# Performance work log

Hardware: AMD Instinct MI355X
Metric: run time of the kernel (lower is better)

## Reference

```python
import jax, jax.numpy as jnp
import numpy as np

D_MODEL = 1024
NUM_HEADS = 16
D_K = D_MODEL // NUM_HEADS
B, S = 2, 2048
NEG = -1.0e9


def setup_inputs() -> dict:
    key = jax.random.key(0)
    ks = jax.random.split(key, 10)
    inp = {
        'query': jax.random.normal(ks[0], (B, S, D_MODEL), dtype=jnp.float32),
        'key':   jax.random.normal(ks[1], (B, S, D_MODEL), dtype=jnp.float32),
        'value': jax.random.normal(ks[2], (B, S, D_MODEL), dtype=jnp.float32),
        'mask':  jax.random.randint(ks[3], (B, S, S), 0, 2, dtype=jnp.int32),
        # nn.Linear params (weight [out,in], bias [out])
        'Wq': jax.random.normal(ks[4], (D_MODEL, D_MODEL), dtype=jnp.float32) * 0.02,
        'bq': jnp.zeros((D_MODEL,), dtype=jnp.float32),
        'Wk': jax.random.normal(ks[5], (D_MODEL, D_MODEL), dtype=jnp.float32) * 0.02,
        'bk': jnp.zeros((D_MODEL,), dtype=jnp.float32),
        'Wv': jax.random.normal(ks[6], (D_MODEL, D_MODEL), dtype=jnp.float32) * 0.02,
        'bv': jnp.zeros((D_MODEL,), dtype=jnp.float32),
    }
    return inp


def reference(query, key, value, mask, Wq, bq, Wk, bk, Wv, bv):
    b = query.shape[0]
    # projections: nn.Linear -> x @ W.T + b
    Q = query @ Wq.T + bq
    K = key @ Wk.T + bk
    V = value @ Wv.T + bv
    # [B, H, S, d_k]
    Q = Q.reshape(b, -1, NUM_HEADS, D_K).transpose(0, 2, 1, 3)
    K = K.reshape(b, -1, NUM_HEADS, D_K).transpose(0, 2, 1, 3)
    V = V.reshape(b, -1, NUM_HEADS, D_K).transpose(0, 2, 1, 3)
    scale = 1.0 / np.sqrt(D_K).astype(np.float32)
    scores = jnp.einsum('bhqd,bhkd->bhqk', Q, K) * scale  # [B,H,S,S]
    scores = jnp.where(mask[:, None, :, :] == 0, NEG, scores)
    attn_weights = jax.nn.softmax(scores, axis=-1)
    out = jnp.einsum('bhqk,bhkd->bhqd', attn_weights, V)
    out = out.transpose(0, 2, 1, 3).reshape(b, -1, D_MODEL)
    return out, attn_weights
```

## Files before the change

kernel.cpp:

```cpp
#include <hip/hip_runtime.h>
#include <hip/hip_bf16.h>
#include <cstdint>
#include <cstddef>

#define S_LEN 2048
#define DM 1024
#define NEGV -1.0e9f

typedef __attribute__((ext_vector_type(8))) short bf16x8;
typedef __attribute__((ext_vector_type(4))) float f32x4;
typedef __attribute__((ext_vector_type(4))) unsigned short us4;
typedef __attribute__((ext_vector_type(4))) int i32x4;
typedef __attribute__((ext_vector_type(4))) unsigned int ui32x4;
typedef __attribute__((ext_vector_type(2))) unsigned int u32x2;

__device__ __forceinline__ unsigned short f2bf(float f) {
  unsigned int u = __float_as_uint(f);
  unsigned int r = (u + 0x7fffu + ((u >> 16) & 1u)) >> 16;
  return (unsigned short)r;
}

__device__ __forceinline__ unsigned int pack_bf2(float a, float b) {
  return (unsigned int)f2bf(a) | ((unsigned int)f2bf(b) << 16);
}

__device__ __forceinline__ void async_copy16(const void* g, void* l) {
  __builtin_amdgcn_global_load_lds((const __attribute__((address_space(1))) void*)g,
                                   (__attribute__((address_space(3))) void*)l, 16, 0, 0);
}

__global__ void cvt_kernel(const float* __restrict__ src, unsigned short* __restrict__ dst, int n4) {
  int i = blockIdx.x * blockDim.x + threadIdx.x;
  if (i >= n4) return;
  const float4 v = reinterpret_cast<const float4*>(src)[i];
  us4 o;
  o[0] = f2bf(v.x); o[1] = f2bf(v.y); o[2] = f2bf(v.z); o[3] = f2bf(v.w);
  reinterpret_cast<us4*>(dst)[i] = o;
}

__global__ __launch_bounds__(256) void maskbits_kernel(const int* __restrict__ mask,
                                                       unsigned int* __restrict__ mb) {
  const int idx = blockIdx.x * 256 + threadIdx.x;
  const int row = idx >> 6, w = idx & 63;
  const int* src = mask + (size_t)row * S_LEN + w * 32;
  unsigned int r = 0;
#pragma unroll
  for (int j = 0; j < 8; ++j) {
    const i32x4 v = *(const i32x4*)(src + j * 4);
    r |= (v[0] ? 1u : 0u) << (j * 4 + 0);
    r |= (v[1] ? 1u : 0u) << (j * 4 + 1);
    r |= (v[2] ? 1u : 0u) << (j * 4 + 2);
    r |= (v[3] ? 1u : 0u) << (j * 4 + 3);
  }
  mb[(size_t)row * 64 + w] = r;
}

__global__ __launch_bounds__(256) void proj_gemm(
    const unsigned short* __restrict__ Xq, const unsigned short* __restrict__ Wqw,
    const float* __restrict__ bq, unsigned short* __restrict__ Cq,
    const unsigned short* __restrict__ Xk, const unsigned short* __restrict__ Wkw,
    const float* __restrict__ bk, unsigned short* __restrict__ Ck,
    const unsigned short* __restrict__ Xv, const unsigned short* __restrict__ Wvw,
    const float* __restrict__ bv, unsigned short* __restrict__ Cv) {
  const unsigned short* X; const unsigned short* W; const float* bias; unsigned short* C;
  if (blockIdx.z == 0)      { X = Xq; W = Wqw; bias = bq; C = Cq; }
  else if (blockIdx.z == 1) { X = Xk; W = Wkw; bias = bk; C = Ck; }
  else                      { X = Xv; W = Wvw; bias = bv; C = Cv; }

  __shared__ unsigned short Ab[128 * 64];
  __shared__ unsigned short Bb[128 * 64];

  const int t  = threadIdx.x;
  const int wv = t >> 6, l = t & 63;
  const int lr = l & 15, lg = l >> 4;
  const int wr = wv >> 1, wc = wv & 1;
  const int m0 = blockIdx.y * 128, n0 = blockIdx.x * 128;

  const f32x4 fz = {0.f, 0.f, 0.f, 0.f};
  f32x4 acc[4][4];
#pragma unroll
  for (int m = 0; m < 4; ++m)
#pragma unroll
    for (int n = 0; n < 4; ++n) acc[m][n] = fz;

  const int srow = t >> 3;
  const int sc16 = t & 7;

  for (int kt = 0; kt < 16; ++kt) {
    const int kb = kt * 64;
#pragma unroll
    for (int it = 0; it < 4; ++it) {
      const int row = it * 32 + srow;
      const int c16 = sc16 ^ (row & 7);
      const unsigned short* gA = X + (size_t)(m0 + row) * DM + kb + c16 * 8;
      const unsigned short* gB = W + (size_t)(n0 + row) * DM + kb + c16 * 8;
      async_copy16(gA, (char*)Ab + it * 4096 + wv * 1024);
      async_copy16(gB, (char*)Bb + it * 4096 + wv * 1024);
    }
    __syncthreads();
#pragma unroll
    for (int kk = 0; kk < 2; ++kk) {
      bf16x8 af[4], bfr[4];
      const int c16 = kk * 4 + lg;
      const int sw = (c16 ^ (lr & 7)) * 16;
#pragma unroll
      for (int m = 0; m < 4; ++m) {
        const int row = wr * 64 + m * 16 + lr;
        af[m] = *(const bf16x8*)((const char*)Ab + row * 128 + sw);
      }
#pragma unroll
      for (int n = 0; n < 4; ++n) {
        const int row = wc * 64 + n * 16 + lr;
        bfr[n] = *(const bf16x8*)((const char*)Bb + row * 128 + sw);
      }
#pragma unroll
      for (int m = 0; m < 4; ++m)
#pragma unroll
        for (int n = 0; n < 4; ++n)
          acc[m][n] = __builtin_amdgcn_mfma_f32_16x16x32_bf16(af[m], bfr[n], acc[m][n], 0, 0, 0);
    }
    __syncthreads();
  }

#pragma unroll
  for (int n = 0; n < 4; ++n) {
    const int ccol = n0 + wc * 64 + n * 16 + lr;
    const float bb = bias[ccol];
#pragma unroll
    for (int m = 0; m < 4; ++m) {
      const int crow0 = m0 + wr * 64 + m * 16 + lg * 4;
#pragma unroll
      for (int j = 0; j < 4; ++j)
        C[(size_t)(crow0 + j) * DM + ccol] = f2bf(acc[m][n][j] + bb);
    }
  }
}

__global__ void transpose_bf(const unsigned short* __restrict__ src, unsigned short* __restrict__ dst) {
  __shared__ unsigned short tb[32][33];
  const int x = threadIdx.x & 31, y = threadIdx.x >> 5;
  const int bx = blockIdx.x, by = blockIdx.y;
#pragma unroll
  for (int r = 0; r < 32; r += 8)
    tb[r + y][x] = src[(size_t)(by * 32 + r + y) * DM + bx * 32 + x];
  __syncthreads();
#pragma unroll
  for (int r = 0; r < 32; r += 8)
    dst[(size_t)(bx * 32 + r + y) * 4096 + by * 32 + x] = tb[x][r + y];
}

__global__ __launch_bounds__(256) void kpack_kernel(const unsigned short* __restrict__ Kp,
                                                    unsigned short* __restrict__ Kpack) {
  const int tid = blockIdx.x * 256 + threadIdx.x;
  const int lane = tid & 63;
  const int chunk = (tid >> 6) & 1;
  const int kb = (tid >> 7) & 127;
  const int h = (tid >> 14) & 15;
  const int b = tid >> 18;
  const unsigned short* src = Kp + (size_t)(b * 2048 + kb * 16 + (lane & 15)) * 1024
                                 + h * 64 + chunk * 32 + (lane >> 4) * 8;
  unsigned short* dst = Kpack + ((size_t)((b * 16 + h) * 128 + kb) * 2 + chunk) * 512 + lane * 8;
  *(bf16x8*)dst = *(const bf16x8*)src;
}

__global__ __launch_bounds__(256) void vpack_kernel(const unsigned short* __restrict__ Vt,
                                                    unsigned short* __restrict__ Vpack) {
  const int tid = blockIdx.x * 256 + threadIdx.x;
  const int lane = tid & 63;
  const int n  = (tid >> 6) & 3;
  const int s2 = (tid >> 8) & 1;
  const int pr = (tid >> 9) & 3;
  const int w  = (tid >> 11) & 7;
  const int h  = (tid >> 14) & 15;
  const int b  = tid >> 18;
  const unsigned short* src = Vt + (size_t)(h * 64 + n * 16 + (lane & 15)) * 4096
                                 + b * 2048 + w * 256 + pr * 64 + s2 * 32 + (lane >> 4) * 8;
  const int blk = ((w * 4 + pr) * 2 + s2) * 4 + n;
  unsigned short* dst = Vpack + ((size_t)(b * 16 + h) * 256 + blk) * 512 + lane * 8;
  *(bf16x8*)dst = *(const bf16x8*)src;
}

__global__ __launch_bounds__(512, 4) void attn15_kernel(
    const unsigned short* __restrict__ Qp, const unsigned short* __restrict__ Kpk,
    const unsigned short* __restrict__ Vpk, const unsigned int* __restrict__ mbits,
    float* __restrict__ outp, float* __restrict__ attnp) {
  __shared__ float rsred[8][16];
  __shared__ float rinv16[16];
  __shared__ char uni[8][4224];

  const int bx = blockIdx.x;
  const int c  = bx & 7;
  const int s  = bx >> 3;
  const int j  = s & 3;
  const int qt = s >> 2;
  const int bh = c * 4 + j;
  const int b  = bh >> 4, h = bh & 15;
  const int q0 = qt << 4;

  const int w = threadIdx.x >> 6, l = threadIdx.x & 63;
  const int lr = l & 15, lg = l >> 4;
  const int kw0 = w << 8;

  const float scale = 0.125f;
  const f32x4 fz = {0.f, 0.f, 0.f, 0.f};

  const unsigned short* Qh = Qp + (size_t)(b * S_LEN + q0 + lr) * DM + h * 64;
  const bf16x8 qf0 = *(const bf16x8*)(Qh + lg * 8);
  const bf16x8 qf1 = *(const bf16x8*)(Qh + 32 + lg * 8);

  const unsigned short* Kw = Kpk + (size_t)((b * 16 + h) * 128 + w * 16) * 1024;

  const unsigned int* mbr = mbits + ((size_t)(b * S_LEN + q0 + lr) << 6) + (kw0 >> 5);
  const ui32x4 mwa = *(const ui32x4*)(mbr);
  const ui32x4 mwb = *(const ui32x4*)(mbr + 4);

  unsigned int pkA[16], pkB[16];
  float rs = 0.f;
#pragma unroll
  for (int i = 0; i < 16; ++i) {
    const bf16x8 ka0 = *(const bf16x8*)(Kw + i * 1024 + l * 8);
    const bf16x8 ka1 = *(const bf16x8*)(Kw + i * 1024 + 512 + l * 8);
    f32x4 sc = fz;
    sc = __builtin_amdgcn_mfma_f32_16x16x32_bf16(ka0, qf0, sc, 0, 0, 0);
    sc = __builtin_amdgcn_mfma_f32_16x16x32_bf16(ka1, qf1, sc, 0, 0, 0);
    const unsigned int wsel = (i < 8) ? mwa[i >> 1] : mwb[(i - 8) >> 1];
    const unsigned int nib = (wsel >> ((i & 1) * 16 + lg * 4)) & 15u;
    const float e0 = __expf((nib & 1u) ? sc[0] * scale : NEGV);
    const float e1 = __expf((nib & 2u) ? sc[1] * scale : NEGV);
    const float e2 = __expf((nib & 4u) ? sc[2] * scale : NEGV);
    const float e3 = __expf((nib & 8u) ? sc[3] * scale : NEGV);
    rs += (e0 + e1) + (e2 + e3);
    pkA[i] = pack_bf2(e0, e1);
    pkB[i] = pack_bf2(e2, e3);
  }
  rs += __shfl_xor(rs, 16, 64);
  rs += __shfl_xor(rs, 32, 64);
  if (l < 16) rsred[w][l] = rs;
  __syncthreads();
  if (threadIdx.x < 16) {
    float s0 = 0.f;
#pragma unroll
    for (int ww = 0; ww < 8; ++ww) s0 += rsred[ww][threadIdx.x];
    rinv16[threadIdx.x] = 1.0f / s0;
  }
  __syncthreads();

  float rv4[4];
#pragma unroll
  for (int i = 0; i < 4; ++i) rv4[i] = rinv16[(l >> 4) + 4 * i];

  float* attnB = attnp + (size_t)((b * 16 + h) * S_LEN + q0) * S_LEN + kw0;
  const unsigned short* Vw = Vpk + ((size_t)(b * 16 + h) * 256 + w * 32) * 512;
  unsigned short* pbase = (unsigned short*)uni[w];

  f32x4 oacc[4];
#pragma unroll
  for (int n = 0; n < 4; ++n) oacc[n] = fz;

#pragma unroll
  for (int pr = 0; pr < 4; ++pr) {
    const int kb = pr * 64;
    unsigned short* pb = pbase + (pr & 1) * 1056;

    bf16x8 vbr[2][4];
#pragma unroll
    for (int s2 = 0; s2 < 2; ++s2)
#pragma unroll
      for (int n = 0; n < 4; ++n)
        vbr[s2][n] = *(const bf16x8*)(Vw + (size_t)(((pr * 2 + s2) * 4) + n) * 512 + l * 8);

#pragma unroll
    for (int s2 = 0; s2 < 2; ++s2) {
      const int wi = pr * 2 + s2;
      const u32x2 wv0 = {pkA[2 * wi],     pkB[2 * wi]};
      const u32x2 wv1 = {pkA[2 * wi + 1], pkB[2 * wi + 1]};
      *(u32x2*)(pb + lr * 66 + s2 * 32 + lg * 4) = wv0;
      *(u32x2*)(pb + lr * 66 + s2 * 32 + 16 + lg * 4) = wv1;
    }
#pragma unroll
    for (int i = 0; i < 4; ++i) {
      const int row = (l >> 4) + i * 4;
      const us4 p4 = *(const us4*)(pb + row * 66 + (l & 15) * 4);
      const float rv = rv4[i];
      const f32x4 st = {__uint_as_float((unsigned)p4[0] << 16) * rv,
                        __uint_as_float((unsigned)p4[1] << 16) * rv,
                        __uint_as_float((unsigned)p4[2] << 16) * rv,
                        __uint_as_float((unsigned)p4[3] << 16) * rv};
      __builtin_nontemporal_store(st, (f32x4*)(attnB + (size_t)row * S_LEN + kb + (l & 15) * 4));
    }
#pragma unroll
    for (int s2 = 0; s2 < 2; ++s2) {
      const bf16x8 pa = *(const bf16x8*)(pb + lr * 66 + s2 * 32 + lg * 8);
#pragma unroll
      for (int n = 0; n < 4; ++n)
        oacc[n] = __builtin_amdgcn_mfma_f32_16x16x32_bf16(pa, vbr[s2][n], oacc[n], 0, 0, 0);
    }
  }

  asm volatile("s_waitcnt lgkmcnt(0)" ::: "memory");
  float* outred = (float*)uni[w];
#pragma unroll
  for (int n = 0; n < 4; ++n)
#pragma unroll
    for (int jj = 0; jj < 4; ++jj)
      outred[(lg * 4 + jj) * 64 + n * 16 + lr] = oacc[n][jj];
  __syncthreads();
  if (threadIdx.x < 256) {
    const int q = threadIdx.x >> 4;
    const int d0 = (threadIdx.x & 15) * 4;
    const float rq = rinv16[q];
    float4 o = {0.f, 0.f, 0.f, 0.f};
#pragma unroll
    for (int ww = 0; ww < 8; ++ww) {
      const f32x4 sv = *(const f32x4*)((const float*)uni[ww] + q * 64 + d0);
      o.x += sv[0]; o.y += sv[1]; o.z += sv[2]; o.w += sv[3];
    }
    o.x *= rq; o.y *= rq; o.z *= rq; o.w *= rq;
    *(float4*)(outp + (size_t)(b * S_LEN + q0 + q) * DM + h * 64 + d0) = o;
  }
}

extern "C" void kernel_launch(void* const* d_in, const int* in_sizes, int n_in,
                              void* d_out, int out_size, void* d_ws, size_t ws_size,
                              hipStream_t stream) {
  const float* query = (const float*)d_in[0];
  const float* key_  = (const float*)d_in[1];
  const float* value = (const float*)d_in[2];
  const int*   mask  = (const int*)d_in[3];
  const float* Wq = (const float*)d_in[4];
  const float* bq = (const float*)d_in[5];
  const float* Wk = (const float*)d_in[6];
  const float* bk = (const float*)d_in[7];
  const float* Wv = (const float*)d_in[8];
  const float* bv = (const float*)d_in[9];

  float* outp  = (float*)d_out;
  float* attnp = outp + (size_t)2 * S_LEN * DM;

  unsigned short* ws  = (unsigned short*)d_ws;
  unsigned short* qbf = ws;
  unsigned short* kbf = qbf + 4194304;
  unsigned short* vbf = kbf + 4194304;
  unsigned short* wqb = vbf + 4194304;
  unsigned short* wkb = wqb + 1048576;
  unsigned short* wvb = wkb + 1048576;
  unsigned short* qp  = wvb + 1048576;
  unsigned short* kp  = qp + 4194304;
  unsigned short* vp  = kp + 4194304;
  unsigned short* vt  = vp + 4194304;
  unsigned int*   mb  = (unsigned int*)(vt + 4194304);
  unsigned short* kpk = qbf;
  unsigned short* vpk = kbf;

  cvt_kernel<<<4096, 256, 0, stream>>>(query, qbf, 1048576);
  cvt_kernel<<<4096, 256, 0, stream>>>(key_,  kbf, 1048576);
  cvt_kernel<<<4096, 256, 0, stream>>>(value, vbf, 1048576);
  cvt_kernel<<<1024, 256, 0, stream>>>(Wq, wqb, 262144);
  cvt_kernel<<<1024, 256, 0, stream>>>(Wk, wkb, 262144);
  cvt_kernel<<<1024, 256, 0, stream>>>(Wv, wvb, 262144);
  maskbits_kernel<<<1024, 256, 0, stream>>>(mask, mb);

  proj_gemm<<<dim3(8, 32, 3), 256, 0, stream>>>(qbf, wqb, bq, qp,
                                                kbf, wkb, bk, kp,
                                                vbf, wvb, bv, vp);
  transpose_bf<<<dim3(32, 128), 256, 0, stream>>>(vp, vt);
  kpack_kernel<<<2048, 256, 0, stream>>>(kp, kpk);
  vpack_kernel<<<2048, 256, 0, stream>>>(vt, vpk);
  attn15_kernel<<<4096, 512, 0, stream>>>(qp, kpk, vpk, mb, outp, attnp);
}
```

Baseline: 256.4 us.

## Fuse conversion launches, remap projection grid, merge V transpose and pack

Merges the six fp32-to-bf16 conversion launches into one kernel. Remaps the projection GEMM to a 1D grid with an XCD-aware block ordering so that blocks sharing an M tile land on the same chiplet. Replaces the separate V transpose and V pack kernels with one kernel that stages a 64x64 tile in LDS and writes the packed MFMA layout directly. This removes launch overhead and one full round trip of V through global memory, in exchange for strided LDS reads in the new pack kernel.

```diff
diff --git a/kernel.cpp b/kernel.cpp
--- a/kernel.cpp
+++ b/kernel.cpp
@@ -29,13 +29,27 @@
                                    (__attribute__((address_space(3))) void*)l, 16, 0, 0);
 }
 
-__global__ void cvt_kernel(const float* __restrict__ src, unsigned short* __restrict__ dst, int n4) {
-  int i = blockIdx.x * blockDim.x + threadIdx.x;
-  if (i >= n4) return;
-  const float4 v = reinterpret_cast<const float4*>(src)[i];
+__global__ __launch_bounds__(256) void cvt_all(
+    const float* __restrict__ q, const float* __restrict__ k, const float* __restrict__ v,
+    const float* __restrict__ wq, const float* __restrict__ wk, const float* __restrict__ wv,
+    unsigned short* __restrict__ qb, unsigned short* __restrict__ kb2, unsigned short* __restrict__ vb,
+    unsigned short* __restrict__ wqb, unsigned short* __restrict__ wkb, unsigned short* __restrict__ wvb) {
+  const int gid = blockIdx.x * 256 + threadIdx.x;
+  const float* src; unsigned short* dst; int idx;
+  if (gid < 3145728) {
+    const int j = gid >> 20; idx = gid & 1048575;
+    src = (j == 0) ? q : (j == 1) ? k : v;
+    dst = (j == 0) ? qb : (j == 1) ? kb2 : vb;
+  } else {
+    const int g = gid - 3145728;
+    const int j = g >> 18; idx = g & 262143;
+    src = (j == 0) ? wq : (j == 1) ? wk : wv;
+    dst = (j == 0) ? wqb : (j == 1) ? wkb : wvb;
+  }
+  const float4 vv = reinterpret_cast<const float4*>(src)[idx];
   us4 o;
-  o[0] = f2bf(v.x); o[1] = f2bf(v.y); o[2] = f2bf(v.z); o[3] = f2bf(v.w);
-  reinterpret_cast<us4*>(dst)[i] = o;
+  o[0] = f2bf(vv.x); o[1] = f2bf(vv.y); o[2] = f2bf(vv.z); o[3] = f2bf(vv.w);
+  reinterpret_cast<us4*>(dst)[idx] = o;
 }
 
 __global__ __launch_bounds__(256) void maskbits_kernel(const int* __restrict__ mask,
@@ -62,19 +76,25 @@
     const float* __restrict__ bk, unsigned short* __restrict__ Ck,
     const unsigned short* __restrict__ Xv, const unsigned short* __restrict__ Wvw,
     const float* __restrict__ bv, unsigned short* __restrict__ Cv) {
+  const int bid = blockIdx.x;
+  const int c = bid & 7, s = bid >> 3;
+  const int n0 = (s & 7) * 128;
+  const int mzg = c * 12 + (s >> 3);
+  const int m0 = (mzg & 31) * 128;
+  const int z = mzg >> 5;
+
   const unsigned short* X; const unsigned short* W; const float* bias; unsigned short* C;
-  if (blockIdx.z == 0)      { X = Xq; W = Wqw; bias = bq; C = Cq; }
-  else if (blockIdx.z == 1) { X = Xk; W = Wkw; bias = bk; C = Ck; }
-  else                      { X = Xv; W = Wvw; bias = bv; C = Cv; }
+  if (z == 0)      { X = Xq; W = Wqw; bias = bq; C = Cq; }
+  else if (z == 1) { X = Xk; W = Wkw; bias = bk; C = Ck; }
+  else             { X = Xv; W = Wvw; bias = bv; C = Cv; }
 
   __shared__ unsigned short Ab[128 * 64];
   __shared__ unsigned short Bb[128 * 64];
 
   const int t  = threadIdx.x;
-  const int wv = t >> 6, l = t & 63;
+  const int wv2 = t >> 6, l = t & 63;
   const int lr = l & 15, lg = l >> 4;
-  const int wr = wv >> 1, wc = wv & 1;
-  const int m0 = blockIdx.y * 128, n0 = blockIdx.x * 128;
+  const int wr = wv2 >> 1, wc = wv2 & 1;
 
   const f32x4 fz = {0.f, 0.f, 0.f, 0.f};
   f32x4 acc[4][4];
@@ -94,8 +114,8 @@
       const int c16 = sc16 ^ (row & 7);
       const unsigned short* gA = X + (size_t)(m0 + row) * DM + kb + c16 * 8;
       const unsigned short* gB = W + (size_t)(n0 + row) * DM + kb + c16 * 8;
-      async_copy16(gA, (char*)Ab + it * 4096 + wv * 1024);
-      async_copy16(gB, (char*)Bb + it * 4096 + wv * 1024);
+      async_copy16(gA, (char*)Ab + it * 4096 + wv2 * 1024);
+      async_copy16(gB, (char*)Bb + it * 4096 + wv2 * 1024);
     }
     __syncthreads();
 #pragma unroll
@@ -134,19 +154,6 @@
         C[(size_t)(crow0 + j) * DM + ccol] = f2bf(acc[m][n][j] + bb);
     }
   }
-}
-
-__global__ void transpose_bf(const unsigned short* __restrict__ src, unsigned short* __restrict__ dst) {
-  __shared__ unsigned short tb[32][33];
-  const int x = threadIdx.x & 31, y = threadIdx.x >> 5;
-  const int bx = blockIdx.x, by = blockIdx.y;
-#pragma unroll
-  for (int r = 0; r < 32; r += 8)
-    tb[r + y][x] = src[(size_t)(by * 32 + r + y) * DM + bx * 32 + x];
-  __syncthreads();
-#pragma unroll
-  for (int r = 0; r < 32; r += 8)
-    dst[(size_t)(bx * 32 + r + y) * 4096 + by * 32 + x] = tb[x][r + y];
 }
 
 __global__ __launch_bounds__(256) void kpack_kernel(const unsigned short* __restrict__ Kp,
@@ -163,24 +170,40 @@
   *(bf16x8*)dst = *(const bf16x8*)src;
 }
 
-__global__ __launch_bounds__(256) void vpack_kernel(const unsigned short* __restrict__ Vt,
-                                                    unsigned short* __restrict__ Vpack) {
-  const int tid = blockIdx.x * 256 + threadIdx.x;
-  const int lane = tid & 63;
-  const int n  = (tid >> 6) & 3;
-  const int s2 = (tid >> 8) & 1;
-  const int pr = (tid >> 9) & 3;
-  const int w  = (tid >> 11) & 7;
-  const int h  = (tid >> 14) & 15;
-  const int b  = tid >> 18;
-  const unsigned short* src = Vt + (size_t)(h * 64 + n * 16 + (lane & 15)) * 4096
-                                 + b * 2048 + w * 256 + pr * 64 + s2 * 32 + (lane >> 4) * 8;
-  const int blk = ((w * 4 + pr) * 2 + s2) * 4 + n;
-  unsigned short* dst = Vpack + ((size_t)(b * 16 + h) * 256 + blk) * 512 + lane * 8;
-  *(bf16x8*)dst = *(const bf16x8*)src;
-}
-
-__global__ __launch_bounds__(512, 4) void attn15_kernel(
+__global__ __launch_bounds__(256) void vtranspack_kernel(const unsigned short* __restrict__ Vp,
+                                                         unsigned short* __restrict__ Vpack) {
+  __shared__ unsigned short tile[64][72];
+  const int id = blockIdx.x;
+  const int pr = id & 3;
+  const int w  = (id >> 2) & 7;
+  const int h  = (id >> 5) & 15;
+  const int b  = id >> 9;
+  const int t  = threadIdx.x;
+  const int R0 = b * 2048 + w * 256 + pr * 64;
+  const int C0 = h * 64;
+  {
+    const int row = t >> 2, q = t & 3;
+    const unsigned short* src = Vp + (size_t)(R0 + row) * 1024 + C0 + q * 16;
+    *(bf16x8*)&tile[row][q * 16] = *(const bf16x8*)src;
+    *(bf16x8*)&tile[row][q * 16 + 8] = *(const bf16x8*)(src + 8);
+  }
+  __syncthreads();
+  unsigned short* dstb = Vpack + ((size_t)(b * 16 + h) * 256 + (w * 4 + pr) * 8) * 512;
+#pragma unroll
+  for (int p2 = 0; p2 < 2; ++p2) {
+    const int cid = p2 * 256 + t;
+    const int blk = cid >> 6;
+    const int lane = cid & 63;
+    const int s2 = blk >> 2, n = blk & 3;
+    unsigned short v[8];
+#pragma unroll
+    for (int e = 0; e < 8; ++e)
+      v[e] = tile[s2 * 32 + (lane >> 4) * 8 + e][n * 16 + (lane & 15)];
+    *(bf16x8*)(dstb + (size_t)blk * 512 + lane * 8) = *(bf16x8*)v;
+  }
+}
+
+__global__ __launch_bounds__(512, 4) void attn16_kernel(
     const unsigned short* __restrict__ Qp, const unsigned short* __restrict__ Kpk,
     const unsigned short* __restrict__ Vpk, const unsigned int* __restrict__ mbits,
     float* __restrict__ outp, float* __restrict__ attnp) {
@@ -347,24 +370,18 @@
   unsigned short* qp  = wvb + 1048576;
   unsigned short* kp  = qp + 4194304;
   unsigned short* vp  = kp + 4194304;
-  unsigned short* vt  = vp + 4194304;
-  unsigned int*   mb  = (unsigned int*)(vt + 4194304);
+  unsigned int*   mb  = (unsigned int*)(vp + 4194304);
   unsigned short* kpk = qbf;
   unsigned short* vpk = kbf;
 
-  cvt_kernel<<<4096, 256, 0, stream>>>(query, qbf, 1048576);
-  cvt_kernel<<<4096, 256, 0, stream>>>(key_,  kbf, 1048576);
-  cvt_kernel<<<4096, 256, 0, stream>>>(value, vbf, 1048576);
-  cvt_kernel<<<1024, 256, 0, stream>>>(Wq, wqb, 262144);
-  cvt_kernel<<<1024, 256, 0, stream>>>(Wk, wkb, 262144);
-  cvt_kernel<<<1024, 256, 0, stream>>>(Wv, wvb, 262144);
+  cvt_all<<<15360, 256, 0, stream>>>(query, key_, value, Wq, Wk, Wv,
+                                     qbf, kbf, vbf, wqb, wkb, wvb);
   maskbits_kernel<<<1024, 256, 0, stream>>>(mask, mb);
 
-  proj_gemm<<<dim3(8, 32, 3), 256, 0, stream>>>(qbf, wqb, bq, qp,
-                                                kbf, wkb, bk, kp,
-                                                vbf, wvb, bv, vp);
-  transpose_bf<<<dim3(32, 128), 256, 0, stream>>>(vp, vt);
+  proj_gemm<<<768, 256, 0, stream>>>(qbf, wqb, bq, qp,
+                                     kbf, wkb, bk, kp,
+                                     vbf, wvb, bv, vp);
   kpack_kernel<<<2048, 256, 0, stream>>>(kp, kpk);
-  vpack_kernel<<<2048, 256, 0, stream>>>(vt, vpk);
-  attn15_kernel<<<4096, 512, 0, stream>>>(qp, kpk, vpk, mb, outp, attnp);
-}
+  vtranspack_kernel<<<1024, 256, 0, stream>>>(vp, vpk);
+  attn16_kernel<<<4096, 512, 0, stream>>>(qp, kpk, vpk, mb, outp, attnp);
+}
```

Measured after the change: 238.3 us. -7.0%, faster.
